# Optimization experiments

Measured on AMD Instinct MI355X. Metric: run time of the kernel, lower is better.

The kernel has to match this reference:

```python
import jax, jax.numpy as jnp
import numpy as np

N0, N1, N2 = 100000, 25000, 6250
E0, E1, E2 = 600000, 150000, 37500
K = 6


def cheb_conv(x, edge_index, W, b):
    """torch_geometric ChebConv with sym normalization, lambda_max=2:
    L_hat = -D^{-1/2} A D^{-1/2}; T0=x, T1=L_hat x, Tk=2 L_hat T_{k-1} - T_{k-2}."""
    n = x.shape[0]
    src, dst = edge_index[0], edge_index[1]
    deg = jax.ops.segment_sum(jnp.ones(src.shape[0], x.dtype), src, num_segments=n)
    dinv = jnp.where(deg > 0, jax.lax.rsqrt(jnp.maximum(deg, 1.0)), 0.0)
    w = -(dinv[src] * dinv[dst])  # [E]

    def prop(h):  # (L_hat h)_i = sum_{j->i} w_ij h_j
        return jax.ops.segment_sum(w[:, None] * h[src], dst, num_segments=n)

    Tx0 = x
    out = Tx0 @ W[0]
    Tx1 = prop(x)
    out = out + Tx1 @ W[1]
    for k in range(2, W.shape[0]):
        Tx2 = 2.0 * prop(Tx1) - Tx0
        out = out + Tx2 @ W[k]
        Tx0, Tx1 = Tx1, Tx2
    return out + b


def pool(x, rows, cols, vals, n_out):
    # sparse.mm(D, x): y[r] += v * x[c]
    return jax.ops.segment_sum(vals[:, None] * x[cols], rows, num_segments=n_out)


def setup_inputs() -> dict:
    key = jax.random.key(0)
    ks = jax.random.split(key, 16)
    inp = {}
    inp["x"] = jax.random.normal(ks[0], (N0, 3), jnp.float32)
    inp["edge_index0"] = jax.random.randint(ks[1], (2, E0), 0, N0, jnp.int32)
    inp["edge_index1"] = jax.random.randint(ks[2], (2, E1), 0, N1, jnp.int32)
    inp["edge_index2"] = jax.random.randint(ks[3], (2, E2), 0, N2, jnp.int32)
    s = 0.05
    inp["W0"] = jax.random.normal(ks[4], (K, 3, 128), jnp.float32) * s
    inp["b0"] = jax.random.normal(ks[5], (128,), jnp.float32) * s
    inp["W1"] = jax.random.normal(ks[6], (K, 128, 128), jnp.float32) * s
    inp["b1"] = jax.random.normal(ks[7], (128,), jnp.float32) * s
    inp["W2"] = jax.random.normal(ks[8], (K, 128, 256), jnp.float32) * s
    inp["b2"] = jax.random.normal(ks[9], (256,), jnp.float32) * s
    inp["D0_rows"] = jax.random.randint(ks[10], (100000,), 0, N1, jnp.int32)
    inp["D0_cols"] = jax.random.randint(ks[11], (100000,), 0, N0, jnp.int32)
    inp["D0_vals"] = jax.random.uniform(ks[12], (100000,), jnp.float32)
    inp["D1_rows"] = jax.random.randint(ks[13], (25000,), 0, N2, jnp.int32)
    inp["D1_cols"] = jax.random.randint(ks[14], (25000,), 0, N1, jnp.int32)
    inp["D1_vals"] = jax.random.uniform(ks[15], (25000,), jnp.float32)
    k2 = jax.random.split(jax.random.fold_in(key, 1), 2)
    inp["linW"] = jax.random.normal(k2[0], (10, N2 * 256), jnp.float32) * 0.001
    inp["linb"] = jax.random.normal(k2[1], (10,), jnp.float32) * s
    return inp


def reference(x, edge_index0, edge_index1, edge_index2, W0, b0, W1, b1, W2, b2,
              D0_rows, D0_cols, D0_vals, D1_rows, D1_cols, D1_vals, linW, linb):
    h = jax.nn.relu(cheb_conv(x, edge_index0, W0, b0))      # [N0,128]
    h = pool(h, D0_rows, D0_cols, D0_vals, N1)               # [N1,128]
    h = jax.nn.relu(cheb_conv(h, edge_index1, W1, b1))      # [N1,128]
    h = pool(h, D1_rows, D1_cols, D1_vals, N2)               # [N2,128]
    h = cheb_conv(h, edge_index2, W2, b2)                    # [N2,256]
    Z = linW @ h.reshape(-1) + linb                           # [10]
    return Z
```

## Files before the change

### kernel.cpp

```cpp
#include <hip/hip_runtime.h>


namespace {
constexpr int cN0 = 100000, cN1 = 25000, cN2 = 6250;
constexpr int cE0 = 600000, cE1 = 150000, cE2 = 37500;
constexpr int cD  = cN2 * 256;

constexpr int JN[5]  = {cN0, cN1, cN2, cN1, cN2};
constexpr int JE[5]  = {cE0, cE1, cE2, 100000, 25000};
constexpr int JB[5]  = {391, 98, 25, 98, 25};
constexpr int JBBASE[6] = {0, 391, 489, 514, 612, 637};
constexpr int TB = 637;
constexpr int JCB[5] = {293, 74, 19, 49, 13};
constexpr int JCBASE[6] = {0, 293, 367, 386, 435, 448};
constexpr int TCB = 448;
constexpr int CHUNK = 2048;
constexpr int BSTRIDE = 400;

constexpr int EBASE[5]   = {0, 600000, 750000, 787500, 887500};
constexpr int E_TOTAL    = 912500;
constexpr int NBASE[5]   = {0, 100096, 125184, 131584, 156672};
constexpr int NPAD_TOTAL = 163072;
constexpr int DEGBASE[3] = {0, 100000, 125000};
constexpr int DEG_TOTAL  = 131250;
constexpr int WPREP_TOTAL = 768 * 128 + 768 * 256 + 128 * 32;
constexpr int PREP_ALL_TOTAL = WPREP_TOTAL + DEG_TOTAL + cN0 + 10;
}

typedef __attribute__((ext_vector_type(8))) short short8;
typedef __attribute__((ext_vector_type(4))) float floatx4;

__device__ inline ushort f2h(float f) {
  union { _Float16 h; ushort u; } v;
  v.h = (_Float16)f;
  return v.u;
}
__device__ inline float h2f(unsigned lo16) {
  union { ushort u; _Float16 h; } v;
  v.u = (ushort)lo16;
  return (float)v.h;
}

__device__ inline int job_of_cb(int cb) {
  int j = 0;
  while (cb >= JCBASE[j + 1]) ++j;
  return j;
}
__device__ inline int job_of_bucket(int g) {
  int j = 0;
  while (g >= JBBASE[j + 1]) ++j;
  return j;
}

__global__ __launch_bounds__(256) void c1_count_kernel(
    const int* __restrict__ k0, const int* __restrict__ k1, const int* __restrict__ k2,
    const int* __restrict__ k3, const int* __restrict__ k4,
    const int* __restrict__ s0, const int* __restrict__ s1, const int* __restrict__ s2,
    int* __restrict__ degcnt, int* __restrict__ cntCB) {
  __shared__ int cnt[BSTRIDE];
  int cb = blockIdx.x;
  int j = job_of_cb(cb);
  int lb = cb - JCBASE[j];
  const int* keys;
  const int* srck = nullptr;
  int dbase = 0;
  switch (j) {
    case 0: keys = k0; srck = s0; dbase = DEGBASE[0]; break;
    case 1: keys = k1; srck = s1; dbase = DEGBASE[1]; break;
    case 2: keys = k2; srck = s2; dbase = DEGBASE[2]; break;
    case 3: keys = k3; break;
    default: keys = k4; break;
  }
  int nB = JB[j];
  for (int b = threadIdx.x; b < nB; b += 256) cnt[b] = 0;
  __syncthreads();
  int e0 = lb * CHUNK;
  int e1 = min(e0 + CHUNK, JE[j]);
  for (int e = e0 + threadIdx.x; e < e1; e += 256) {
    atomicAdd(&cnt[keys[e] >> 8], 1);
    if (srck) atomicAdd(&degcnt[dbase + srck[e]], 1);
  }
  __syncthreads();
  for (int b = threadIdx.x; b < nB; b += 256)
    cntCB[cb * BSTRIDE + b] = cnt[b];
}

__global__ __launch_bounds__(256) void c2a_scan_kernel(int* __restrict__ cntCB,
                                                       int* __restrict__ bucketTot,
                                                       const int* __restrict__ degcnt,
                                                       float* __restrict__ dinv) {
  __shared__ int s[256];
  int g = blockIdx.x;
  int j = job_of_bucket(g);
  int b = g - JBBASE[j];
  int cb0 = JCBASE[j], nCB = JCB[j];
  int carry = 0;
  for (int c0 = 0; c0 < nCB; c0 += 256) {
    int i = c0 + threadIdx.x;
    int v = (i < nCB) ? cntCB[(cb0 + i) * BSTRIDE + b] : 0;
    s[threadIdx.x] = v;
    __syncthreads();
    for (int d = 1; d < 256; d <<= 1) {
      int t = (threadIdx.x >= d) ? s[threadIdx.x - d] : 0;
      __syncthreads();
      s[threadIdx.x] += t;
      __syncthreads();
    }
    if (i < nCB) cntCB[(cb0 + i) * BSTRIDE + b] = carry + s[threadIdx.x] - v;
    carry += s[255];
    __syncthreads();
  }
  if (threadIdx.x == 0) bucketTot[g] = carry;
  int idx = blockIdx.x * 256 + threadIdx.x;
  if (idx < DEG_TOTAL) {
    int c = degcnt[idx];
    dinv[idx] = (c > 0) ? rsqrtf((float)c) : 0.f;
  }
}

__global__ __launch_bounds__(256) void c2b_scan_kernel(const int* __restrict__ bucketTot,
                                                       int* __restrict__ bucketBase) {
  __shared__ int s[256];
  int j = blockIdx.x;
  int g0 = JBBASE[j], nB = JB[j];
  int carry = 0;
  for (int c0 = 0; c0 < nB; c0 += 256) {
    int i = c0 + threadIdx.x;
    int v = (i < nB) ? bucketTot[g0 + i] : 0;
    s[threadIdx.x] = v;
    __syncthreads();
    for (int d = 1; d < 256; d <<= 1) {
      int t = (threadIdx.x >= d) ? s[threadIdx.x - d] : 0;
      __syncthreads();
      s[threadIdx.x] += t;
      __syncthreads();
    }
    if (i < nB) bucketBase[g0 + i] = carry + s[threadIdx.x] - v;
    carry += s[255];
    __syncthreads();
  }
}

__global__ __launch_bounds__(256) void c3_dst_kernel(
    const int* __restrict__ d0, const int* __restrict__ s0,
    const int* __restrict__ d1, const int* __restrict__ s1,
    const int* __restrict__ d2, const int* __restrict__ s2,
    const int* __restrict__ p0r, const int* __restrict__ p0c, const float* __restrict__ p0v,
    const int* __restrict__ p1r, const int* __restrict__ p1c, const float* __restrict__ p1v,
    const float* __restrict__ dinv,
    const int* __restrict__ cntCB, const int* __restrict__ bucketBase,
    int2* __restrict__ scatPairs) {
  __shared__ int base[BSTRIDE];
  int cb = blockIdx.x;
  int j = job_of_cb(cb);
  int lb = cb - JCBASE[j];
  const int* dk; const int* sk; const float* vv = nullptr;
  switch (j) {
    case 0: dk = d0; sk = s0; break;
    case 1: dk = d1; sk = s1; break;
    case 2: dk = d2; sk = s2; break;
    case 3: dk = p0r; sk = p0c; vv = p0v; break;
    default: dk = p1r; sk = p1c; vv = p1v; break;
  }
  int nB = JB[j];
  for (int b = threadIdx.x; b < nB; b += 256)
    base[b] = EBASE[j] + bucketBase[JBBASE[j] + b] + cntCB[cb * BSTRIDE + b];
  __syncthreads();
  int e0 = lb * CHUNK;
  int e1 = min(e0 + CHUNK, JE[j]);
  for (int e = e0 + threadIdx.x; e < e1; e += 256) {
    int d = dk[e];
    int s = sk[e];
    float w;
    if (j < 3) w = -(dinv[DEGBASE[j] + s] * dinv[DEGBASE[j] + d]);
    else w = vv[e];
    int pos = atomicAdd(&base[d >> 8], 1);
    scatPairs[pos] = make_int2(((d & 255) << 17) | s, __float_as_int(w));
  }
}

__global__ __launch_bounds__(256) void dcsr_kernel(const int2* __restrict__ scatPairs,
                                                   const int* __restrict__ bucketTot,
                                                   const int* __restrict__ bucketBase,
                                                   int* __restrict__ off,
                                                   int2* __restrict__ csrPairs) {
  __shared__ int cnt[256];
  __shared__ int sArr[256];
  __shared__ int cur[256];
  int g = blockIdx.x;
  int j = job_of_bucket(g);
  int b = g - JBBASE[j];
  int relBase = bucketBase[g];
  int st = EBASE[j] + relBase;
  int en = st + bucketTot[g];
  cnt[threadIdx.x] = 0;
  __syncthreads();
  for (int idx = st + threadIdx.x; idx < en; idx += 256)
    atomicAdd(&cnt[scatPairs[idx].x >> 17], 1);
  __syncthreads();
  int v = cnt[threadIdx.x];
  sArr[threadIdx.x] = v;
  __syncthreads();
  for (int d = 1; d < 256; d <<= 1) {
    int t = (threadIdx.x >= d) ? sArr[threadIdx.x - d] : 0;
    __syncthreads();
    sArr[threadIdx.x] += t;
    __syncthreads();
  }
  int excl = sArr[threadIdx.x] - v;
  int node = b * 256 + threadIdx.x;
  if (node < JN[j]) off[NBASE[j] + node] = relBase + excl;
  if (threadIdx.x == 0 && b == JB[j] - 1) off[NBASE[j] + JN[j]] = JE[j];
  cur[threadIdx.x] = st + excl;
  __syncthreads();
  for (int idx = st + threadIdx.x; idx < en; idx += 256) {
    int2 p = scatPairs[idx];
    int dl = p.x >> 17;
    int s = p.x & 0x1FFFF;
    int pos = atomicAdd(&cur[dl], 1);
    csrPairs[pos] = make_int2(s, p.y);
  }
}

__global__ __launch_bounds__(256) void csr_prop128h_kernel(
    const int* __restrict__ off, const int2* __restrict__ pairs,
    const ushort* __restrict__ hh, float* __restrict__ y, ushort* __restrict__ yh,
    const float* __restrict__ prev, float scale, int N) {
  int r = blockIdx.x * 8 + (threadIdx.x >> 5);
  int l = threadIdx.x & 31;
  if (r >= N) return;
  int s = off[r], e = off[r + 1];
  const uint2* h2 = (const uint2*)hh;
  float ax = 0.f, ay = 0.f, az = 0.f, aw = 0.f;
  int j = s;
  for (; j + 4 <= e; j += 4) {
    int2 p0 = pairs[j], p1 = pairs[j + 1], p2 = pairs[j + 2], p3 = pairs[j + 3];
    uint2 v0 = h2[(size_t)p0.x * 32 + l];
    uint2 v1 = h2[(size_t)p1.x * 32 + l];
    uint2 v2 = h2[(size_t)p2.x * 32 + l];
    uint2 v3 = h2[(size_t)p3.x * 32 + l];
    float w0 = __int_as_float(p0.y), w1 = __int_as_float(p1.y);
    float w2 = __int_as_float(p2.y), w3 = __int_as_float(p3.y);
    ax += w0 * h2f(v0.x & 0xFFFFu) + w1 * h2f(v1.x & 0xFFFFu)
        + w2 * h2f(v2.x & 0xFFFFu) + w3 * h2f(v3.x & 0xFFFFu);
    ay += w0 * h2f(v0.x >> 16) + w1 * h2f(v1.x >> 16)
        + w2 * h2f(v2.x >> 16) + w3 * h2f(v3.x >> 16);
    az += w0 * h2f(v0.y & 0xFFFFu) + w1 * h2f(v1.y & 0xFFFFu)
        + w2 * h2f(v2.y & 0xFFFFu) + w3 * h2f(v3.y & 0xFFFFu);
    aw += w0 * h2f(v0.y >> 16) + w1 * h2f(v1.y >> 16)
        + w2 * h2f(v2.y >> 16) + w3 * h2f(v3.y >> 16);
  }
  for (; j < e; ++j) {
    int2 p = pairs[j];
    uint2 v0 = h2[(size_t)p.x * 32 + l];
    float w = __int_as_float(p.y);
    ax += w * h2f(v0.x & 0xFFFFu);
    ay += w * h2f(v0.x >> 16);
    az += w * h2f(v0.y & 0xFFFFu);
    aw += w * h2f(v0.y >> 16);
  }
  float4 v = make_float4(scale * ax, scale * ay, scale * az, scale * aw);
  if (prev) {
    float4 pv = ((const float4*)prev)[(size_t)r * 32 + l];
    v.x -= pv.x; v.y -= pv.y; v.z -= pv.z; v.w -= pv.w;
  }
  if (y) ((float4*)y)[(size_t)r * 32 + l] = v;
  uint2 sp = make_uint2(f2h(v.x) | ((unsigned)f2h(v.y) << 16),
                        f2h(v.z) | ((unsigned)f2h(v.w) << 16));
  ((uint2*)yh)[(size_t)r * 32 + l] = sp;
}

__global__ void csr_prop3_kernel(const int* __restrict__ off, const int2* __restrict__ pairs,
                                 const float4* __restrict__ h, float4* __restrict__ y,
                                 const float4* __restrict__ prev, float scale, int N,
                                 ushort* __restrict__ yh, int kout) {
  int r = blockIdx.x * blockDim.x + threadIdx.x;
  if (r >= N) return;
  int s = off[r], e = off[r + 1];
  float ax = 0.f, ay = 0.f, az = 0.f;
  int j = s;
  for (; j + 4 <= e; j += 4) {
    int2 p0 = pairs[j], p1 = pairs[j + 1], p2 = pairs[j + 2], p3 = pairs[j + 3];
    float4 h0 = h[p0.x], h1 = h[p1.x], h2 = h[p2.x], h3 = h[p3.x];
    float w0 = __int_as_float(p0.y), w1 = __int_as_float(p1.y);
    float w2 = __int_as_float(p2.y), w3 = __int_as_float(p3.y);
    ax += w0 * h0.x + w1 * h1.x + w2 * h2.x + w3 * h3.x;
    ay += w0 * h0.y + w1 * h1.y + w2 * h2.y + w3 * h3.y;
    az += w0 * h0.z + w1 * h1.z + w2 * h2.z + w3 * h3.z;
  }
  for (; j < e; ++j) {
    int2 p = pairs[j];
    float4 hv = h[p.x];
    float w = __int_as_float(p.y);
    ax += w * hv.x; ay += w * hv.y; az += w * hv.z;
  }
  float4 v = make_float4(scale * ax, scale * ay, scale * az, 0.f);
  if (prev) {
    float4 pv = prev[r];
    v.x -= pv.x; v.y -= pv.y; v.z -= pv.z;
  }
  y[r] = v;
  uint2 sp = make_uint2(f2h(v.x) | ((unsigned)f2h(v.y) << 16), (unsigned)f2h(v.z));
  *(uint2*)(yh + (size_t)r * 32 + kout * 4) = sp;
}

__global__ __launch_bounds__(256, 2) void h0_mfma_kernel(
    const ushort* __restrict__ Ah, const ushort* __restrict__ W0h,
    const float* __restrict__ b0, ushort* __restrict__ h0h, int M) {
  __shared__ ushort Al[64][40];
  __shared__ ushort Bl[128][40];
  __shared__ ushort Hs[64][128];
  const int tid = threadIdx.x;
  const int rowBase = blockIdx.x * 64;
  const int wave = tid >> 6;
  const int lane = tid & 63;
  const int m16 = lane & 15;
  const int quad = lane >> 4;
  {
    int sRow = tid >> 2;
    int sK8 = (tid & 3) * 8;
    int row = rowBase + sRow;
    uint4 av = make_uint4(0, 0, 0, 0);
    if (row < M) av = *(const uint4*)(Ah + (size_t)row * 32 + sK8);
    *(uint4*)&Al[sRow][sK8] = av;
  }
#pragma unroll
  for (int l = 0; l < 2; ++l) {
    int lin = tid + l * 256;
    int bRow = lin >> 2;
    int bK8 = (lin & 3) * 8;
    *(uint4*)&Bl[bRow][bK8] = *(const uint4*)(W0h + (size_t)bRow * 32 + bK8);
  }
  __syncthreads();
  short8 a = *(const short8*)&Al[wave * 16 + m16][quad * 8];
  floatx4 acc[8];
#pragma unroll
  for (int c = 0; c < 8; ++c) {
    floatx4 z;
    z[0] = 0.f; z[1] = 0.f; z[2] = 0.f; z[3] = 0.f;
    short8 b = *(const short8*)&Bl[c * 16 + m16][quad * 8];
    acc[c] = __builtin_amdgcn_mfma_f32_16x16x32_f16(a, b, z, 0, 0, 0);
  }
#pragma unroll
  for (int c = 0; c < 8; ++c) {
    int col = c * 16 + m16;
    float bv = b0[col];
#pragma unroll
    for (int r = 0; r < 4; ++r)
      Hs[wave * 16 + quad * 4 + r][col] = f2h(fmaxf(acc[c][r] + bv, 0.f));
  }
  __syncthreads();
  const uint4* ls = (const uint4*)&Hs[0][0];
  uint4* gd = (uint4*)(h0h + (size_t)rowBase * 128);
#pragma unroll
  for (int i = 0; i < 4; ++i) {
    int idx = tid + i * 256;
    if (rowBase + (idx >> 4) < M) gd[idx] = ls[idx];
  }
}

__global__ void prep_all_kernel(const float* __restrict__ W0, const float* __restrict__ W1,
                                const float* __restrict__ W2, ushort* __restrict__ W0h,
                                ushort* __restrict__ Wt1, ushort* __restrict__ Wt2,
                                int* __restrict__ degcnt,
                                const float* __restrict__ x, float4* __restrict__ Tb,
                                ushort* __restrict__ Ah,
                                float* __restrict__ out, const float* __restrict__ linb) {
  int i = blockIdx.x * 256 + threadIdx.x;
  if (i < 768 * 128) {
    int k = i / 128, n = i - k * 128;
    Wt1[(size_t)n * 768 + k] = f2h(W1[i]);
  } else if (i < 768 * 128 + 768 * 256) {
    int i2 = i - 768 * 128;
    int k = i2 / 256, n = i2 - k * 256;
    Wt2[(size_t)n * 768 + k] = f2h(W2[i2]);
  } else if (i < WPREP_TOTAL) {
    int i3 = i - 768 * 128 - 768 * 256;
    int col = i3 >> 5, k = i3 & 31;
    int a = k >> 2, jj = k & 3;
    float v = (k < 24 && jj < 3) ? W0[(a * 3 + jj) * 128 + col] : 0.f;
    W0h[(size_t)col * 32 + k] = f2h(v);
  } else if (i < WPREP_TOTAL + DEG_TOTAL) {
    degcnt[i - WPREP_TOTAL] = 0;
  } else if (i < WPREP_TOTAL + DEG_TOTAL + cN0) {
    int r = i - (WPREP_TOTAL + DEG_TOTAL);
    float x0 = x[3 * r], x1 = x[3 * r + 1], x2 = x[3 * r + 2];
    Tb[r] = make_float4(x0, x1, x2, 0.f);
    uint4 z = make_uint4(0, 0, 0, 0);
    uint4 first = make_uint4(f2h(x0) | ((unsigned)f2h(x1) << 16), (unsigned)f2h(x2), 0, 0);
    uint4* p = (uint4*)(Ah + (size_t)r * 32);
    p[0] = first; p[1] = z; p[2] = z; p[3] = z;
  } else if (i < PREP_ALL_TOTAL) {
    int o = i - (WPREP_TOTAL + DEG_TOTAL + cN0);
    out[o] = linb[o];
  }
}

template <int RELU, int OUTH>
__global__ __launch_bounds__(256, 2) void gemm_mfma_kernel(
    const ushort* __restrict__ Th, const ushort* __restrict__ Wt,
    const float* __restrict__ bias, float* __restrict__ C, ushort* __restrict__ Ch,
    int M, int N) {
  __shared__ ushort Al[64][40];
  __shared__ ushort Bl[128][40];
  __shared__ ushort Hs[64][128];
  const int tid = threadIdx.x;
  const int rowBase = blockIdx.x * 64;
  const int colBase = blockIdx.y * 128;
  const int wave = tid >> 6;
  const int lane = tid & 63;
  const int m16 = lane & 15;
  const int quad = lane >> 4;
  const size_t Mstride = (size_t)M * 128;

  floatx4 acc[8];
#pragma unroll
  for (int c = 0; c < 8; ++c)
#pragma unroll
    for (int r = 0; r < 4; ++r) acc[c][r] = 0.f;

  const int sRow = tid >> 2;
  const int sK8 = (tid & 3) * 8;
  const int growA = rowBase + sRow;
  const bool aValid = growA < M;

  for (int kc = 0; kc < 24; ++kc) {
    uint4 av = make_uint4(0, 0, 0, 0);
    if (aValid)
      av = *(const uint4*)(Th + (size_t)(kc >> 2) * Mstride + (size_t)growA * 128
                           + ((kc & 3) << 5) + sK8);
    *(uint4*)&Al[sRow][sK8] = av;
#pragma unroll
    for (int l = 0; l < 2; ++l) {
      int lin = tid + l * 256;
      int bRow = lin >> 2;
      int bK8 = (lin & 3) * 8;
      *(uint4*)&Bl[bRow][bK8] =
          *(const uint4*)(Wt + (size_t)(colBase + bRow) * 768 + kc * 32 + bK8);
    }
    __syncthreads();

    short8 a = *(const short8*)&Al[wave * 16 + m16][quad * 8];
#pragma unroll
    for (int c = 0; c < 8; ++c) {
      short8 b = *(const short8*)&Bl[c * 16 + m16][quad * 8];
      acc[c] = __builtin_amdgcn_mfma_f32_16x16x32_f16(a, b, acc[c], 0, 0, 0);
    }
    __syncthreads();
  }

  if (OUTH) {
#pragma unroll
    for (int c = 0; c < 8; ++c) {
      int col = c * 16 + m16;
      float bv = bias[col];
#pragma unroll
      for (int r = 0; r < 4; ++r) {
        float v = acc[c][r] + bv;
        if (RELU) v = fmaxf(v, 0.f);
        Hs[wave * 16 + quad * 4 + r][col] = f2h(v);
      }
    }
    __syncthreads();
    const uint4* ls = (const uint4*)&Hs[0][0];
    uint4* gd = (uint4*)(Ch + (size_t)rowBase * 128);
#pragma unroll
    for (int i = 0; i < 4; ++i) {
      int idx = tid + i * 256;
      if (rowBase + (idx >> 4) < M) gd[idx] = ls[idx];
    }
  } else {
#pragma unroll
    for (int c = 0; c < 8; ++c) {
      int col = colBase + c * 16 + m16;
      float bv = bias[col];
#pragma unroll
      for (int r = 0; r < 4; ++r) {
        int row = rowBase + wave * 16 + quad * 4 + r;
        if (row < M) {
          float v = acc[c][r] + bv;
          if (RELU) v = fmaxf(v, 0.f);
          C[(size_t)row * N + col] = v;
        }
      }
    }
  }
}

__global__ __launch_bounds__(256) void linear_kernel(const float* __restrict__ Wl,
                                                     const float* __restrict__ h,
                                                     float* __restrict__ out, int D) {
  float p[10];
#pragma unroll
  for (int j = 0; j < 10; ++j) p[j] = 0.f;
  int stride = gridDim.x * blockDim.x;
  for (int i = blockIdx.x * blockDim.x + threadIdx.x; i < D; i += stride) {
    float hv = h[i];
#pragma unroll
    for (int j = 0; j < 10; ++j) p[j] += Wl[(size_t)j * D + i] * hv;
  }
#pragma unroll
  for (int j = 0; j < 10; ++j) {
#pragma unroll
    for (int off = 32; off > 0; off >>= 1) p[j] += __shfl_down(p[j], off, 64);
  }
  __shared__ float s[4][10];
  int wave = threadIdx.x >> 6, lane = threadIdx.x & 63;
  if (lane == 0) {
#pragma unroll
    for (int j = 0; j < 10; ++j) s[wave][j] = p[j];
  }
  __syncthreads();
  if (threadIdx.x < 10) {
    float t = s[0][threadIdx.x] + s[1][threadIdx.x] + s[2][threadIdx.x] + s[3][threadIdx.x];
    atomicAdd(&out[threadIdx.x], t);
  }
}

extern "C" void kernel_launch(void* const* d_in, const int* in_sizes, int n_in,
                              void* d_out, int out_size, void* d_ws, size_t ws_size,
                              hipStream_t stream) {
  const float* x    = (const float*)d_in[0];
  const int*   ei0  = (const int*)d_in[1];
  const int*   ei1  = (const int*)d_in[2];
  const int*   ei2  = (const int*)d_in[3];
  const float* W0   = (const float*)d_in[4];
  const float* b0   = (const float*)d_in[5];
  const float* W1   = (const float*)d_in[6];
  const float* b1   = (const float*)d_in[7];
  const float* W2   = (const float*)d_in[8];
  const float* b2   = (const float*)d_in[9];
  const int*   D0r  = (const int*)d_in[10];
  const int*   D0c  = (const int*)d_in[11];
  const float* D0v  = (const float*)d_in[12];
  const int*   D1r  = (const int*)d_in[13];
  const int*   D1c  = (const int*)d_in[14];
  const float* D1v  = (const float*)d_in[15];
  const float* linW = (const float*)d_in[16];
  const float* linb = (const float*)d_in[17];
  float* out = (float*)d_out;
  (void)in_sizes; (void)n_in; (void)out_size; (void)ws_size;

  const int* src0 = ei0;            const int* dst0 = ei0 + cE0;
  const int* src1 = ei1;            const int* dst1 = ei1 + cE1;
  const int* src2 = ei2;            const int* dst2 = ei2 + cE2;

  float* ws = (float*)d_ws;
  size_t off = 0;
  auto alloc = [&](size_t n) {
    float* p = ws + off;
    off += (n + 63) & ~size_t(63);
    return p;
  };
  float* dinv       = alloc(DEG_TOTAL);
  int*   degcnt     = (int*)alloc(DEG_TOTAL);
  int*   cntCB      = (int*)alloc((size_t)TCB * BSTRIDE);
  int*   bucketTot  = (int*)alloc(TB);
  int*   bucketBase = (int*)alloc(TB);
  int2*  scatPairs  = (int2*)alloc((size_t)2 * E_TOTAL);
  int2*  csrPairs   = (int2*)alloc((size_t)2 * E_TOTAL);
  int*   offArr     = (int*)alloc(NPAD_TOTAL);
  ushort* W0h       = (ushort*)alloc(128 * 32 / 2);
  ushort* Wt1       = (ushort*)alloc(768 * 128 / 2);
  ushort* Wt2       = (ushort*)alloc(768 * 256 / 2);
  float4* Tb0       = (float4*)alloc((size_t)6 * cN0 * 4);
  ushort* Ah0       = (ushort*)alloc((size_t)cN0 * 16);
  ushort* h0h       = (ushort*)alloc((size_t)cN0 * 64);
  float* Tlvl1      = alloc((size_t)6 * cN1 * 128);
  ushort* Th1       = (ushort*)alloc((size_t)6 * cN1 * 64);
  ushort* out1h     = (ushort*)alloc((size_t)cN1 * 64);
  float* Tlvl2      = alloc((size_t)6 * cN2 * 128);
  ushort* Th2       = (ushort*)alloc((size_t)6 * cN2 * 64);
  float* out2       = alloc((size_t)cN2 * 256);

  auto nb = [](long long n) { return (unsigned)((n + 255) / 256); };

  prep_all_kernel<<<nb(PREP_ALL_TOTAL), 256, 0, stream>>>(
      W0, W1, W2, W0h, Wt1, Wt2, degcnt, x, Tb0, Ah0, out, linb);

  c1_count_kernel<<<TCB, 256, 0, stream>>>(dst0, dst1, dst2, D0r, D1r,
                                           src0, src1, src2, degcnt, cntCB);
  c2a_scan_kernel<<<TB, 256, 0, stream>>>(cntCB, bucketTot, degcnt, dinv);
  c2b_scan_kernel<<<5, 256, 0, stream>>>(bucketTot, bucketBase);
  c3_dst_kernel<<<TCB, 256, 0, stream>>>(dst0, src0, dst1, src1, dst2, src2,
                                         D0r, D0c, D0v, D1r, D1c, D1v,
                                         dinv, cntCB, bucketBase, scatPairs);
  dcsr_kernel<<<TB, 256, 0, stream>>>(scatPairs, bucketTot, bucketBase,
                                      offArr, csrPairs);

  auto seg_off   = [&](int s) { return offArr + NBASE[s]; };
  auto seg_pairs = [&](int s) { return csrPairs + EBASE[s]; };

  {
    auto Tk = [&](int k) { return Tb0 + (size_t)k * cN0; };
    csr_prop3_kernel<<<nb(cN0), 256, 0, stream>>>(seg_off(0), seg_pairs(0),
        Tk(0), Tk(1), nullptr, 1.f, cN0, Ah0, 1);
    csr_prop3_kernel<<<nb(cN0), 256, 0, stream>>>(seg_off(0), seg_pairs(0),
        Tk(1), Tk(2), Tk(0), 2.f, cN0, Ah0, 2);
    csr_prop3_kernel<<<nb(cN0), 256, 0, stream>>>(seg_off(0), seg_pairs(0),
        Tk(2), Tk(3), Tk(1), 2.f, cN0, Ah0, 3);
    csr_prop3_kernel<<<nb(cN0), 256, 0, stream>>>(seg_off(0), seg_pairs(0),
        Tk(3), Tk(4), Tk(2), 2.f, cN0, Ah0, 4);
    csr_prop3_kernel<<<nb(cN0), 256, 0, stream>>>(seg_off(0), seg_pairs(0),
        Tk(4), Tk(5), Tk(3), 2.f, cN0, Ah0, 5);
  }
  h0_mfma_kernel<<<(cN0 + 63) / 64, 256, 0, stream>>>(Ah0, W0h, b0, h0h, cN0);
  csr_prop128h_kernel<<<(cN1 + 7) / 8, 256, 0, stream>>>(
      seg_off(3), seg_pairs(3), h0h, Tlvl1, Th1, nullptr, 1.f, cN1);

  {
    auto Tk  = [&](int k) { return Tlvl1 + (size_t)k * cN1 * 128; };
    auto Thk = [&](int k) { return Th1 + (size_t)k * cN1 * 128; };
    auto prop = [&](int kin, int kout, int kprev, float scale, bool needF32) {
      csr_prop128h_kernel<<<(cN1 + 7) / 8, 256, 0, stream>>>(
          seg_off(1), seg_pairs(1), Thk(kin), needF32 ? Tk(kout) : nullptr, Thk(kout),
          (kprev >= 0) ? Tk(kprev) : nullptr, scale, cN1);
    };
    prop(0, 1, -1, 1.f, true);
    prop(1, 2, 0, 2.f, true);
    prop(2, 3, 1, 2.f, true);
    prop(3, 4, 2, 2.f, true);
    prop(4, 5, 3, 2.f, false);
    dim3 g((cN1 + 63) / 64, 1);
    gemm_mfma_kernel<1, 1><<<g, 256, 0, stream>>>(Th1, Wt1, b1, nullptr, out1h,
                                                  cN1, 128);
  }

  csr_prop128h_kernel<<<(cN2 + 7) / 8, 256, 0, stream>>>(
      seg_off(4), seg_pairs(4), out1h, Tlvl2, Th2, nullptr, 1.f, cN2);

  {
    auto Tk  = [&](int k) { return Tlvl2 + (size_t)k * cN2 * 128; };
    auto Thk = [&](int k) { return Th2 + (size_t)k * cN2 * 128; };
    auto prop = [&](int kin, int kout, int kprev, float scale, bool needF32) {
      csr_prop128h_kernel<<<(cN2 + 7) / 8, 256, 0, stream>>>(
          seg_off(2), seg_pairs(2), Thk(kin), needF32 ? Tk(kout) : nullptr, Thk(kout),
          (kprev >= 0) ? Tk(kprev) : nullptr, scale, cN2);
    };
    prop(0, 1, -1, 1.f, true);
    prop(1, 2, 0, 2.f, true);
    prop(2, 3, 1, 2.f, true);
    prop(3, 4, 2, 2.f, true);
    prop(4, 5, 3, 2.f, false);
    dim3 g((cN2 + 63) / 64, 2);
    gemm_mfma_kernel<0, 0><<<g, 256, 0, stream>>>(Th2, Wt2, b2, out2, nullptr,
                                                  cN2, 256);
  }

  linear_kernel<<<512, 256, 0, stream>>>(linW, out2, out, cD);
}
```

Measured before the change: 418.8 us.

## Replace two-pass bucket CSR build with per-node atomic count-scan-scatter; split 3-wide prop rows

CSR construction no longer does a coarse bucket histogram followed by a second per-bucket local sort. It now counts edges per destination node with global atomics, scans the counts hierarchically, and scatters pairs directly using per-node atomic cursors. This removes the scatPairs intermediate and the dcsr pass, at the cost of more global atomic contention and nondeterministic edge order within each row. Separately, the 3-channel propagation kernel assigns four threads per row and combines their partial sums with shuffles, to spread the gather latency across more lanes.

```diff
diff --git a/kernel.cpp b/kernel.cpp
--- a/kernel.cpp
+++ b/kernel.cpp
@@ -15,7 +15,6 @@
 constexpr int JCBASE[6] = {0, 293, 367, 386, 435, 448};
 constexpr int TCB = 448;
 constexpr int CHUNK = 2048;
-constexpr int BSTRIDE = 400;
 
 constexpr int EBASE[5]   = {0, 600000, 750000, 787500, 887500};
 constexpr int E_TOTAL    = 912500;
@@ -24,7 +23,7 @@
 constexpr int DEGBASE[3] = {0, 100000, 125000};
 constexpr int DEG_TOTAL  = 131250;
 constexpr int WPREP_TOTAL = 768 * 128 + 768 * 256 + 128 * 32;
-constexpr int PREP_ALL_TOTAL = WPREP_TOTAL + DEG_TOTAL + cN0 + 10;
+constexpr int PREP_ALL_TOTAL = WPREP_TOTAL + DEG_TOTAL + NPAD_TOTAL + cN0 + 10;
 }
 
 typedef __attribute__((ext_vector_type(8))) short short8;
@@ -56,8 +55,7 @@
     const int* __restrict__ k0, const int* __restrict__ k1, const int* __restrict__ k2,
     const int* __restrict__ k3, const int* __restrict__ k4,
     const int* __restrict__ s0, const int* __restrict__ s1, const int* __restrict__ s2,
-    int* __restrict__ degcnt, int* __restrict__ cntCB) {
-  __shared__ int cnt[BSTRIDE];
+    int* __restrict__ degcnt, int* __restrict__ nodecnt) {
   int cb = blockIdx.x;
   int j = job_of_cb(cb);
   int lb = cb - JCBASE[j];
@@ -71,33 +69,51 @@
     case 3: keys = k3; break;
     default: keys = k4; break;
   }
-  int nB = JB[j];
-  for (int b = threadIdx.x; b < nB; b += 256) cnt[b] = 0;
-  __syncthreads();
+  int nb = NBASE[j];
   int e0 = lb * CHUNK;
   int e1 = min(e0 + CHUNK, JE[j]);
   for (int e = e0 + threadIdx.x; e < e1; e += 256) {
-    atomicAdd(&cnt[keys[e] >> 8], 1);
+    atomicAdd(&nodecnt[nb + keys[e]], 1);
     if (srck) atomicAdd(&degcnt[dbase + srck[e]], 1);
   }
-  __syncthreads();
-  for (int b = threadIdx.x; b < nB; b += 256)
-    cntCB[cb * BSTRIDE + b] = cnt[b];
-}
-
-__global__ __launch_bounds__(256) void c2a_scan_kernel(int* __restrict__ cntCB,
-                                                       int* __restrict__ bucketTot,
-                                                       const int* __restrict__ degcnt,
-                                                       float* __restrict__ dinv) {
+}
+
+__global__ __launch_bounds__(256) void s1_scan_kernel(
+    const int* __restrict__ nodecnt, int* __restrict__ offArr,
+    int* __restrict__ blockTot,
+    const int* __restrict__ degcnt, float* __restrict__ dinv) {
   __shared__ int s[256];
   int g = blockIdx.x;
   int j = job_of_bucket(g);
   int b = g - JBBASE[j];
-  int cb0 = JCBASE[j], nCB = JCB[j];
+  int idx = NBASE[j] + b * 256 + threadIdx.x;
+  int v = nodecnt[idx];
+  s[threadIdx.x] = v;
+  __syncthreads();
+  for (int d = 1; d < 256; d <<= 1) {
+    int t = (threadIdx.x >= d) ? s[threadIdx.x - d] : 0;
+    __syncthreads();
+    s[threadIdx.x] += t;
+    __syncthreads();
+  }
+  offArr[idx] = s[threadIdx.x] - v;
+  if (threadIdx.x == 0) blockTot[g] = s[255];
+  int di = blockIdx.x * 256 + threadIdx.x;
+  if (di < DEG_TOTAL) {
+    int c = degcnt[di];
+    dinv[di] = (c > 0) ? rsqrtf((float)c) : 0.f;
+  }
+}
+
+__global__ __launch_bounds__(256) void s2_scan_kernel(const int* __restrict__ blockTot,
+                                                      int* __restrict__ blockBase) {
+  __shared__ int s[256];
+  int j = blockIdx.x;
+  int g0 = JBBASE[j], nB = JB[j];
   int carry = 0;
-  for (int c0 = 0; c0 < nCB; c0 += 256) {
+  for (int c0 = 0; c0 < nB; c0 += 256) {
     int i = c0 + threadIdx.x;
-    int v = (i < nCB) ? cntCB[(cb0 + i) * BSTRIDE + b] : 0;
+    int v = (i < nB) ? blockTot[g0 + i] : 0;
     s[threadIdx.x] = v;
     __syncthreads();
     for (int d = 1; d < 256; d <<= 1) {
@@ -106,51 +122,33 @@
       s[threadIdx.x] += t;
       __syncthreads();
     }
-    if (i < nCB) cntCB[(cb0 + i) * BSTRIDE + b] = carry + s[threadIdx.x] - v;
+    if (i < nB) blockBase[g0 + i] = carry + s[threadIdx.x] - v;
     carry += s[255];
     __syncthreads();
   }
-  if (threadIdx.x == 0) bucketTot[g] = carry;
-  int idx = blockIdx.x * 256 + threadIdx.x;
-  if (idx < DEG_TOTAL) {
-    int c = degcnt[idx];
-    dinv[idx] = (c > 0) ? rsqrtf((float)c) : 0.f;
-  }
-}
-
-__global__ __launch_bounds__(256) void c2b_scan_kernel(const int* __restrict__ bucketTot,
-                                                       int* __restrict__ bucketBase) {
-  __shared__ int s[256];
-  int j = blockIdx.x;
-  int g0 = JBBASE[j], nB = JB[j];
-  int carry = 0;
-  for (int c0 = 0; c0 < nB; c0 += 256) {
-    int i = c0 + threadIdx.x;
-    int v = (i < nB) ? bucketTot[g0 + i] : 0;
-    s[threadIdx.x] = v;
-    __syncthreads();
-    for (int d = 1; d < 256; d <<= 1) {
-      int t = (threadIdx.x >= d) ? s[threadIdx.x - d] : 0;
-      __syncthreads();
-      s[threadIdx.x] += t;
-      __syncthreads();
-    }
-    if (i < nB) bucketBase[g0 + i] = carry + s[threadIdx.x] - v;
-    carry += s[255];
-    __syncthreads();
-  }
-}
-
-__global__ __launch_bounds__(256) void c3_dst_kernel(
+}
+
+__global__ __launch_bounds__(256) void s3_fix_kernel(int* __restrict__ offArr,
+                                                     int* __restrict__ cursor,
+                                                     const int* __restrict__ blockBase) {
+  int g = blockIdx.x;
+  int j = job_of_bucket(g);
+  int b = g - JBBASE[j];
+  int idx = NBASE[j] + b * 256 + threadIdx.x;
+  int v = offArr[idx] + blockBase[g];
+  offArr[idx] = v;
+  cursor[idx] = v;
+  if (threadIdx.x == 0 && b == JB[j] - 1) offArr[NBASE[j] + JN[j]] = JE[j];
+}
+
+__global__ __launch_bounds__(256) void scatter_kernel(
     const int* __restrict__ d0, const int* __restrict__ s0,
     const int* __restrict__ d1, const int* __restrict__ s1,
     const int* __restrict__ d2, const int* __restrict__ s2,
     const int* __restrict__ p0r, const int* __restrict__ p0c, const float* __restrict__ p0v,
     const int* __restrict__ p1r, const int* __restrict__ p1c, const float* __restrict__ p1v,
     const float* __restrict__ dinv,
-    const int* __restrict__ cntCB, const int* __restrict__ bucketBase,
-    int2* __restrict__ scatPairs) {
-  __shared__ int base[BSTRIDE];
+    int* __restrict__ cursor, int2* __restrict__ csrPairs) {
   int cb = blockIdx.x;
   int j = job_of_cb(cb);
   int lb = cb - JCBASE[j];
@@ -162,10 +160,8 @@
     case 3: dk = p0r; sk = p0c; vv = p0v; break;
     default: dk = p1r; sk = p1c; vv = p1v; break;
   }
-  int nB = JB[j];
-  for (int b = threadIdx.x; b < nB; b += 256)
-    base[b] = EBASE[j] + bucketBase[JBBASE[j] + b] + cntCB[cb * BSTRIDE + b];
-  __syncthreads();
+  int nb = NBASE[j];
+  int eb = EBASE[j];
   int e0 = lb * CHUNK;
   int e1 = min(e0 + CHUNK, JE[j]);
   for (int e = e0 + threadIdx.x; e < e1; e += 256) {
@@ -174,51 +170,8 @@
     float w;
     if (j < 3) w = -(dinv[DEGBASE[j] + s] * dinv[DEGBASE[j] + d]);
     else w = vv[e];
-    int pos = atomicAdd(&base[d >> 8], 1);
-    scatPairs[pos] = make_int2(((d & 255) << 17) | s, __float_as_int(w));
-  }
-}
-
-__global__ __launch_bounds__(256) void dcsr_kernel(const int2* __restrict__ scatPairs,
-                                                   const int* __restrict__ bucketTot,
-                                                   const int* __restrict__ bucketBase,
-                                                   int* __restrict__ off,
-                                                   int2* __restrict__ csrPairs) {
-  __shared__ int cnt[256];
-  __shared__ int sArr[256];
-  __shared__ int cur[256];
-  int g = blockIdx.x;
-  int j = job_of_bucket(g);
-  int b = g - JBBASE[j];
-  int relBase = bucketBase[g];
-  int st = EBASE[j] + relBase;
-  int en = st + bucketTot[g];
-  cnt[threadIdx.x] = 0;
-  __syncthreads();
-  for (int idx = st + threadIdx.x; idx < en; idx += 256)
-    atomicAdd(&cnt[scatPairs[idx].x >> 17], 1);
-  __syncthreads();
-  int v = cnt[threadIdx.x];
-  sArr[threadIdx.x] = v;
-  __syncthreads();
-  for (int d = 1; d < 256; d <<= 1) {
-    int t = (threadIdx.x >= d) ? sArr[threadIdx.x - d] : 0;
-    __syncthreads();
-    sArr[threadIdx.x] += t;
-    __syncthreads();
-  }
-  int excl = sArr[threadIdx.x] - v;
-  int node = b * 256 + threadIdx.x;
-  if (node < JN[j]) off[NBASE[j] + node] = relBase + excl;
-  if (threadIdx.x == 0 && b == JB[j] - 1) off[NBASE[j] + JN[j]] = JE[j];
-  cur[threadIdx.x] = st + excl;
-  __syncthreads();
-  for (int idx = st + threadIdx.x; idx < en; idx += 256) {
-    int2 p = scatPairs[idx];
-    int dl = p.x >> 17;
-    int s = p.x & 0x1FFFF;
-    int pos = atomicAdd(&cur[dl], 1);
-    csrPairs[pos] = make_int2(s, p.y);
+    int pos = atomicAdd(&cursor[nb + d], 1);
+    csrPairs[eb + pos] = make_int2(s, __float_as_int(w));
   }
 }
 
@@ -270,38 +223,35 @@
   ((uint2*)yh)[(size_t)r * 32 + l] = sp;
 }
 
-__global__ void csr_prop3_kernel(const int* __restrict__ off, const int2* __restrict__ pairs,
-                                 const float4* __restrict__ h, float4* __restrict__ y,
-                                 const float4* __restrict__ prev, float scale, int N,
-                                 ushort* __restrict__ yh, int kout) {
-  int r = blockIdx.x * blockDim.x + threadIdx.x;
+__global__ __launch_bounds__(256) void csr_prop3_kernel(
+    const int* __restrict__ off, const int2* __restrict__ pairs,
+    const float4* __restrict__ h, float4* __restrict__ y,
+    const float4* __restrict__ prev, float scale, int N,
+    ushort* __restrict__ yh, int kout) {
+  int t = blockIdx.x * 256 + threadIdx.x;
+  int r = t >> 2;
+  int q = t & 3;
   if (r >= N) return;
   int s = off[r], e = off[r + 1];
   float ax = 0.f, ay = 0.f, az = 0.f;
-  int j = s;
-  for (; j + 4 <= e; j += 4) {
-    int2 p0 = pairs[j], p1 = pairs[j + 1], p2 = pairs[j + 2], p3 = pairs[j + 3];
-    float4 h0 = h[p0.x], h1 = h[p1.x], h2 = h[p2.x], h3 = h[p3.x];
-    float w0 = __int_as_float(p0.y), w1 = __int_as_float(p1.y);
-    float w2 = __int_as_float(p2.y), w3 = __int_as_float(p3.y);
-    ax += w0 * h0.x + w1 * h1.x + w2 * h2.x + w3 * h3.x;
-    ay += w0 * h0.y + w1 * h1.y + w2 * h2.y + w3 * h3.y;
-    az += w0 * h0.z + w1 * h1.z + w2 * h2.z + w3 * h3.z;
-  }
-  for (; j < e; ++j) {
+  for (int j = s + q; j < e; j += 4) {
     int2 p = pairs[j];
     float4 hv = h[p.x];
     float w = __int_as_float(p.y);
     ax += w * hv.x; ay += w * hv.y; az += w * hv.z;
   }
-  float4 v = make_float4(scale * ax, scale * ay, scale * az, 0.f);
-  if (prev) {
-    float4 pv = prev[r];
-    v.x -= pv.x; v.y -= pv.y; v.z -= pv.z;
-  }
-  y[r] = v;
-  uint2 sp = make_uint2(f2h(v.x) | ((unsigned)f2h(v.y) << 16), (unsigned)f2h(v.z));
-  *(uint2*)(yh + (size_t)r * 32 + kout * 4) = sp;
+  ax += __shfl_xor(ax, 1); ay += __shfl_xor(ay, 1); az += __shfl_xor(az, 1);
+  ax += __shfl_xor(ax, 2); ay += __shfl_xor(ay, 2); az += __shfl_xor(az, 2);
+  if (q == 0) {
+    float4 v = make_float4(scale * ax, scale * ay, scale * az, 0.f);
+    if (prev) {
+      float4 pv = prev[r];
+      v.x -= pv.x; v.y -= pv.y; v.z -= pv.z;
+    }
+    y[r] = v;
+    uint2 sp = make_uint2(f2h(v.x) | ((unsigned)f2h(v.y) << 16), (unsigned)f2h(v.z));
+    *(uint2*)(yh + (size_t)r * 32 + kout * 4) = sp;
+  }
 }
 
 __global__ __launch_bounds__(256, 2) void h0_mfma_kernel(
@@ -362,7 +312,7 @@
 __global__ void prep_all_kernel(const float* __restrict__ W0, const float* __restrict__ W1,
                                 const float* __restrict__ W2, ushort* __restrict__ W0h,
                                 ushort* __restrict__ Wt1, ushort* __restrict__ Wt2,
-                                int* __restrict__ degcnt,
+                                int* __restrict__ degcnt, int* __restrict__ nodecnt,
                                 const float* __restrict__ x, float4* __restrict__ Tb,
                                 ushort* __restrict__ Ah,
                                 float* __restrict__ out, const float* __restrict__ linb) {
@@ -382,8 +332,10 @@
     W0h[(size_t)col * 32 + k] = f2h(v);
   } else if (i < WPREP_TOTAL + DEG_TOTAL) {
     degcnt[i - WPREP_TOTAL] = 0;
-  } else if (i < WPREP_TOTAL + DEG_TOTAL + cN0) {
-    int r = i - (WPREP_TOTAL + DEG_TOTAL);
+  } else if (i < WPREP_TOTAL + DEG_TOTAL + NPAD_TOTAL) {
+    nodecnt[i - (WPREP_TOTAL + DEG_TOTAL)] = 0;
+  } else if (i < WPREP_TOTAL + DEG_TOTAL + NPAD_TOTAL + cN0) {
+    int r = i - (WPREP_TOTAL + DEG_TOTAL + NPAD_TOTAL);
     float x0 = x[3 * r], x1 = x[3 * r + 1], x2 = x[3 * r + 2];
     Tb[r] = make_float4(x0, x1, x2, 0.f);
     uint4 z = make_uint4(0, 0, 0, 0);
@@ -391,7 +343,7 @@
     uint4* p = (uint4*)(Ah + (size_t)r * 32);
     p[0] = first; p[1] = z; p[2] = z; p[3] = z;
   } else if (i < PREP_ALL_TOTAL) {
-    int o = i - (WPREP_TOTAL + DEG_TOTAL + cN0);
+    int o = i - (WPREP_TOTAL + DEG_TOTAL + NPAD_TOTAL + cN0);
     out[o] = linb[o];
   }
 }
@@ -554,10 +506,10 @@
   };
   float* dinv       = alloc(DEG_TOTAL);
   int*   degcnt     = (int*)alloc(DEG_TOTAL);
-  int*   cntCB      = (int*)alloc((size_t)TCB * BSTRIDE);
-  int*   bucketTot  = (int*)alloc(TB);
-  int*   bucketBase = (int*)alloc(TB);
-  int2*  scatPairs  = (int2*)alloc((size_t)2 * E_TOTAL);
+  int*   nodecnt    = (int*)alloc(NPAD_TOTAL);
+  int*   cursor     = (int*)alloc(NPAD_TOTAL);
+  int*   blockTot   = (int*)alloc(TB);
+  int*   blockBase  = (int*)alloc(TB);
   int2*  csrPairs   = (int2*)alloc((size_t)2 * E_TOTAL);
   int*   offArr     = (int*)alloc(NPAD_TOTAL);
   ushort* W0h       = (ushort*)alloc(128 * 32 / 2);
@@ -576,32 +528,31 @@
   auto nb = [](long long n) { return (unsigned)((n + 255) / 256); };
 
   prep_all_kernel<<<nb(PREP_ALL_TOTAL), 256, 0, stream>>>(
-      W0, W1, W2, W0h, Wt1, Wt2, degcnt, x, Tb0, Ah0, out, linb);
+      W0, W1, W2, W0h, Wt1, Wt2, degcnt, nodecnt, x, Tb0, Ah0, out, linb);
 
   c1_count_kernel<<<TCB, 256, 0, stream>>>(dst0, dst1, dst2, D0r, D1r,
-                                           src0, src1, src2, degcnt, cntCB);
-  c2a_scan_kernel<<<TB, 256, 0, stream>>>(cntCB, bucketTot, degcnt, dinv);
-  c2b_scan_kernel<<<5, 256, 0, stream>>>(bucketTot, bucketBase);
-  c3_dst_kernel<<<TCB, 256, 0, stream>>>(dst0, src0, dst1, src1, dst2, src2,
-                                         D0r, D0c, D0v, D1r, D1c, D1v,
-                                         dinv, cntCB, bucketBase, scatPairs);
-  dcsr_kernel<<<TB, 256, 0, stream>>>(scatPairs, bucketTot, bucketBase,
-                                      offArr, csrPairs);
+                                           src0, src1, src2, degcnt, nodecnt);
+  s1_scan_kernel<<<TB, 256, 0, stream>>>(nodecnt, offArr, blockTot, degcnt, dinv);
+  s2_scan_kernel<<<5, 256, 0, stream>>>(blockTot, blockBase);
+  s3_fix_kernel<<<TB, 256, 0, stream>>>(offArr, cursor, blockBase);
+  scatter_kernel<<<TCB, 256, 0, stream>>>(dst0, src0, dst1, src1, dst2, src2,
+                                          D0r, D0c, D0v, D1r, D1c, D1v,
+                                          dinv, cursor, csrPairs);
 
   auto seg_off   = [&](int s) { return offArr + NBASE[s]; };
   auto seg_pairs = [&](int s) { return csrPairs + EBASE[s]; };
 
   {
     auto Tk = [&](int k) { return Tb0 + (size_t)k * cN0; };
-    csr_prop3_kernel<<<nb(cN0), 256, 0, stream>>>(seg_off(0), seg_pairs(0),
+    csr_prop3_kernel<<<nb((size_t)4 * cN0), 256, 0, stream>>>(seg_off(0), seg_pairs(0),
         Tk(0), Tk(1), nullptr, 1.f, cN0, Ah0, 1);
-    csr_prop3_kernel<<<nb(cN0), 256, 0, stream>>>(seg_off(0), seg_pairs(0),
+    csr_prop3_kernel<<<nb((size_t)4 * cN0), 256, 0, stream>>>(seg_off(0), seg_pairs(0),
         Tk(1), Tk(2), Tk(0), 2.f, cN0, Ah0, 2);
-    csr_prop3_kernel<<<nb(cN0), 256, 0, stream>>>(seg_off(0), seg_pairs(0),
+    csr_prop3_kernel<<<nb((size_t)4 * cN0), 256, 0, stream>>>(seg_off(0), seg_pairs(0),
         Tk(2), Tk(3), Tk(1), 2.f, cN0, Ah0, 3);
-    csr_prop3_kernel<<<nb(cN0), 256, 0, stream>>>(seg_off(0), seg_pairs(0),
+    csr_prop3_kernel<<<nb((size_t)4 * cN0), 256, 0, stream>>>(seg_off(0), seg_pairs(0),
         Tk(3), Tk(4), Tk(2), 2.f, cN0, Ah0, 4);
-    csr_prop3_kernel<<<nb(cN0), 256, 0, stream>>>(seg_off(0), seg_pairs(0),
+    csr_prop3_kernel<<<nb((size_t)4 * cN0), 256, 0, stream>>>(seg_off(0), seg_pairs(0),
         Tk(4), Tk(5), Tk(3), 2.f, cN0, Ah0, 5);
   }
   h0_mfma_kernel<<<(cN0 + 63) / 64, 256, 0, stream>>>(Ah0, W0h, b0, h0h, cN0);
```

New measurement: 482.9 us. +15.3%, slower.
